# Kernel optimization log

Hardware: AMD Instinct MI355X
Metric: run time of the kernel (lower is better)

The kernel has to match this reference:

```python
import jax, jax.numpy as jnp
import numpy as np

V, D, H, L, F, B, S = 512, 512, 8, 6, 2048, 8, 1024
DK = D // H
EPS = 1e-5


def _positional_encoding(max_len, d_model):
    pos = np.arange(max_len, dtype=np.float32)[:, None]
    div = np.exp(np.arange(0, d_model, 2, dtype=np.float32) * (-np.log(10000.0) / d_model))
    pe = np.zeros((max_len, d_model), dtype=np.float32)
    pe[:, 0::2] = np.sin(pos * div)
    pe[:, 1::2] = np.cos(pos * div)
    return jnp.asarray(pe)


def setup_inputs() -> dict:
    key = jax.random.key(0)
    ks = jax.random.split(key, 24)
    xavier = lambda k, shp: jax.random.normal(k, shp, jnp.float32) * np.sqrt(2.0 / (shp[-2] + shp[-1]))
    inp = {
        "input_ids": jax.random.randint(ks[0], (B, S), 0, V),
        "emb": jax.random.normal(ks[1], (V, D), jnp.float32) * 0.02,
        "pe": _positional_encoding(1024, D),
        "Wq": xavier(ks[2], (L, D, D)), "bq": jnp.zeros((L, D)),
        "Wk": xavier(ks[3], (L, D, D)), "bk": jnp.zeros((L, D)),
        "Wv": xavier(ks[4], (L, D, D)), "bv": jnp.zeros((L, D)),
        "Wo": xavier(ks[5], (L, D, D)), "bo": jnp.zeros((L, D)),
        "ln1_g": jnp.ones((L, D)), "ln1_b": jnp.zeros((L, D)),
        "W1": xavier(ks[6], (L, D, F)), "b1": jnp.zeros((L, F)),
        "W2": xavier(ks[7], (L, F, D)), "b2": jnp.zeros((L, D)),
        "ln2_g": jnp.ones((L, D)), "ln2_b": jnp.zeros((L, D)),
        "Wout": xavier(ks[8], (D, V)), "bout": jnp.zeros((V,)),
    }
    return inp


def _ln(x, g, b):
    mu = jnp.mean(x, -1, keepdims=True)
    var = jnp.mean(jnp.square(x - mu), -1, keepdims=True)
    return (x - mu) * jax.lax.rsqrt(var + EPS) * g + b


def reference(input_ids, emb, pe, Wq, bq, Wk, bk, Wv, bv, Wo, bo,
              ln1_g, ln1_b, W1, b1, W2, b2, ln2_g, ln2_b, Wout, bout):
    h = emb[input_ids] * np.sqrt(D) + pe[:S]  # [B,S,D]
    # Faithful to the original mask bug: masked_fill(mask==0, -1e9) fills the
    # LOWER triangle (incl diagonal); raw scores are kept strictly where j > i.
    r = jnp.arange(S)
    keep = r[None, :] > r[:, None]  # [S,S]

    def block(h, p):
        (wq, bq_, wk, bk_, wv, bv_, wo, bo_,
         g1, be1, w1, b1_, w2, b2_, g2, be2) = p
        split = lambda t: t.reshape(B, S, H, DK).transpose(0, 2, 1, 3)
        q = split(h @ wq + bq_)
        k = split(h @ wk + bk_)
        v = split(h @ wv + bv_)
        scores = jnp.einsum('bhqd,bhkd->bhqk', q, k) / np.sqrt(DK)
        scores = jnp.where(keep, scores, -1e9)
        a = jax.nn.softmax(scores, axis=-1)
        o = jnp.einsum('bhqk,bhkd->bhqd', a, v).transpose(0, 2, 1, 3).reshape(B, S, D)
        h = _ln(h + (o @ wo + bo_), g1, be1)
        f = jax.nn.relu(h @ w1 + b1_) @ w2 + b2_
        h = _ln(h + f, g2, be2)
        return h, None

    params = (Wq, bq, Wk, bk, Wv, bv, Wo, bo, ln1_g, ln1_b, W1, b1, W2, b2, ln2_g, ln2_b)
    h, _ = jax.lax.scan(block, h, params)
    return h @ Wout + bout  # logits [B,S,V]
```

## Files before the change

kernel.cpp:

```cpp
#include <hip/hip_runtime.h>

typedef unsigned short u16;
typedef __attribute__((ext_vector_type(8))) short bf16x8;
typedef __attribute__((ext_vector_type(4))) float f32x4;
typedef __attribute__((ext_vector_type(4))) unsigned int uint4v;
typedef __attribute__((ext_vector_type(4))) unsigned short us4;

#define NLAYER 6
#define D_MODEL 512
#define NHEAD 8
#define DKH 64
#define SEQ 1024
#define BATCH 8
#define FFN 2048
#define MROWS (BATCH * SEQ)
#define QKV_LD 1536
#define SCALE_LOG2E 0.18033688011112042f

__device__ __forceinline__ float b2f(u16 u) {
  union { unsigned u32; float f; } x; x.u32 = ((unsigned)u) << 16; return x.f;
}
__device__ __forceinline__ u16 f2b(float f) {
  union { float f; unsigned u; } x; x.f = f;
  unsigned r = x.u + 0x7FFFu + ((x.u >> 16) & 1u);
  return (u16)(r >> 16);
}
__device__ __forceinline__ void gld16(const u16* g, u16* l) {
  __builtin_amdgcn_global_load_lds(
      (const __attribute__((address_space(1))) unsigned int*)g,
      (__attribute__((address_space(3))) unsigned int*)l, 16, 0, 0);
}

__global__ __launch_bounds__(256) void transpose_cvt_kernel(
    const float* __restrict__ src, u16* __restrict__ dst, int K, int N, size_t dstZ,
    float scale)
{
  __shared__ float t[32][33];
  const int z = blockIdx.z;
  src += (size_t)z * K * N;
  dst += (size_t)z * dstZ;
  const int n0 = blockIdx.x * 32, k0 = blockIdx.y * 32;
  const int tx = threadIdx.x, ty = threadIdx.y;
#pragma unroll
  for (int i = 0; i < 32; i += 8)
    t[ty + i][tx] = src[(size_t)(k0 + ty + i) * N + n0 + tx];
  __syncthreads();
#pragma unroll
  for (int i = 0; i < 32; i += 8)
    dst[(size_t)(n0 + ty + i) * K + k0 + tx] = f2b(t[tx][ty + i] * scale);
}

__global__ __launch_bounds__(256) void concat_bias_kernel(
    const float* __restrict__ bq, const float* __restrict__ bk,
    const float* __restrict__ bv, float* __restrict__ dst)
{
  const int l = blockIdx.x, t = threadIdx.x;
#pragma unroll
  for (int j = t; j < 512; j += 256) {
    dst[l * QKV_LD + j]        = bq[l * 512 + j] * SCALE_LOG2E;
    dst[l * QKV_LD + 512 + j]  = bk[l * 512 + j];
    dst[l * QKV_LD + 1024 + j] = bv[l * 512 + j];
  }
}

__global__ __launch_bounds__(256) void embed_kernel(
    const int* __restrict__ ids, const float* __restrict__ emb,
    const float* __restrict__ pe, float* __restrict__ Hf, u16* __restrict__ Hb)
{
  const int row = blockIdx.x;
  const int s = row & (SEQ - 1);
  const int id = ids[row];
  const int tid = threadIdx.x;
#pragma unroll
  for (int u = 0; u < 2; ++u) {
    const int d = tid + u * 256;
    float v = emb[(size_t)id * D_MODEL + d] * 22.62741699796952f + pe[(size_t)s * D_MODEL + d];
    Hf[(size_t)row * D_MODEL + d] = v;
    Hb[(size_t)row * D_MODEL + d] = f2b(v);
  }
}

template<int BMT, bool RELU, bool OUTF, bool OUTB, bool VT>
__global__ __launch_bounds__(256) void gemm_kernel(
    const u16* __restrict__ A, const u16* __restrict__ Bt,
    const float* __restrict__ bias,
    float* __restrict__ Cf, u16* __restrict__ Cb, u16* __restrict__ Vtp,
    int M, int N, int K)
{
  constexpr int IT = BMT / 32;
  constexpr int AHALF = BMT * 64;
  constexpr int BHALF = 128 * 64;
  __shared__ __align__(16) u16 As[2 * AHALF];
  __shared__ __align__(16) u16 Bs[2 * BHALF];
  const int tid = threadIdx.x;
  const int bm = blockIdx.x * BMT, bn = blockIdx.y * 128;
  const int wave = tid >> 6, lane = tid & 63;
  const int lm = lane & 15, quad = lane >> 4;
  const int wm = (wave & 1) * (BMT / 2), wn = (wave >> 1) * 64;

  const int sr = tid >> 3;
  const int sc = (tid & 7) ^ (sr & 7);
  const u16* Ap = A  + (size_t)(bm + sr) * K + sc * 8;
  const u16* Bp = Bt + (size_t)(bn + sr) * K + sc * 8;
  u16* lA = As + wave * 512;
  u16* lB = Bs + wave * 512;

  f32x4 acc[IT][4] = {};

  const int nt = K >> 6;
  auto stage = [&](int buf, int t) {
    const size_t ko = (size_t)t << 6;
#pragma unroll
    for (int p = 0; p < BMT / 32; ++p)
      gld16(Ap + (size_t)(p * 32) * K + ko, lA + buf * AHALF + p * 2048);
#pragma unroll
    for (int p = 0; p < 4; ++p)
      gld16(Bp + (size_t)(p * 32) * K + ko, lB + buf * BHALF + p * 2048);
  };

  stage(0, 0);
  __syncthreads();

  for (int t = 0; t < nt; ++t) {
    const int cur = t & 1;
    if (t + 1 < nt) stage(cur ^ 1, t + 1);
    const u16* as = As + cur * AHALF;
    const u16* bs = Bs + cur * BHALF;
#pragma unroll
    for (int kh = 0; kh < 2; ++kh) {
      bf16x8 af[IT], bg[4];
#pragma unroll
      for (int i = 0; i < IT; ++i) {
        const int row = wm + i * 16 + lm;
        af[i] = *(const bf16x8*)&as[row * 64 + (((kh * 4 + quad) ^ (row & 7)) << 3)];
      }
#pragma unroll
      for (int j = 0; j < 4; ++j) {
        const int row = wn + j * 16 + lm;
        bg[j] = *(const bf16x8*)&bs[row * 64 + (((kh * 4 + quad) ^ (row & 7)) << 3)];
      }
#pragma unroll
      for (int i = 0; i < IT; ++i)
#pragma unroll
        for (int j = 0; j < 4; ++j)
          acc[i][j] = __builtin_amdgcn_mfma_f32_16x16x32_bf16(af[i], bg[j], acc[i][j], 0, 0, 0);
    }
    __syncthreads();
  }

  const int mbase = bm + wm + quad * 4;
  const int nbase = bn + wn + lm;
#pragma unroll
  for (int i = 0; i < IT; ++i) {
#pragma unroll
    for (int j = 0; j < 4; ++j) {
      const int n = nbase + j * 16;
      const float bv = bias[n];
      float vv[4];
#pragma unroll
      for (int r = 0; r < 4; ++r) {
        float v = acc[i][j][r] + bv;
        if (RELU) v = fmaxf(v, 0.f);
        vv[r] = v;
      }
      if (VT && n >= 1024) {
        const int hh = (n - 1024) >> 6, d = (n - 1024) & 63;
        const int mm = mbase + i * 16;
        const int bb = mm >> 10, ss = mm & 1023;
        us4 pk;
#pragma unroll
        for (int r = 0; r < 4; ++r) pk[r] = f2b(vv[r]);
        *(us4*)&Vtp[(((size_t)(bb * NHEAD + hh)) * 64 + d) * SEQ + ss] = pk;
      } else {
#pragma unroll
        for (int r = 0; r < 4; ++r) {
          const int m = mbase + i * 16 + r;
          if (OUTF) Cf[(size_t)m * N + n] = vv[r];
          if (OUTB) Cb[(size_t)m * N + n] = f2b(vv[r]);
        }
      }
    }
  }
}

__global__ __launch_bounds__(256) void attn_mfma_kernel(
    const u16* __restrict__ QKV, const u16* __restrict__ Vt, u16* __restrict__ O)
{
  __shared__ __align__(16) u16 Ks[64 * 64];
  __shared__ __align__(16) u16 Vs[64 * 64];
  __shared__ __align__(16) u16 Ps[4 * 16 * 64];
  const int tid = threadIdx.x;
  const int wave = tid >> 6, lane = tid & 63;
  const int quad = lane >> 4, l15 = lane & 15;
  const int l7 = l15 & 7;
  const int id = blockIdx.x;
  const int bh = id & 63;
  const int b = bh >> 3, h = bh & 7;
  const int g = id >> 6;
  const int u = g * 4 + wave;
  u16* psw = Ps + wave * (16 * 64);
  const size_t qoff = (size_t)b * SEQ * QKV_LD + h * 64;
  const size_t vtb  = (size_t)bh * 64 * SEQ;

  const int sr = tid >> 3, sc = tid & 7;
  const u16* kg0 = QKV + qoff + 512 + (size_t)sr * QKV_LD + sc * 8;
  const u16* kg1 = kg0 + (size_t)32 * QKV_LD;
  const u16* vg0 = Vt + vtb + (size_t)sr * SEQ + sc * 8;
  const u16* vg1 = vg0 + (size_t)32 * SEQ;
  const int sw = (sc ^ (sr & 7)) << 3;
  u16* ks0 = &Ks[sr * 64 + sw];
  u16* ks1 = &Ks[(sr + 32) * 64 + sw];
  u16* vs0 = &Vs[sr * 64 + sw];
  u16* vs1 = &Vs[(sr + 32) * 64 + sw];

  const u16* qp = QKV + qoff + (size_t)(u * 16 + l15) * QKV_LD + quad * 8;
  const bf16x8 qf0 = *(const bf16x8*)(qp);
  const bf16x8 qf1 = *(const bf16x8*)(qp + 32);

  f32x4 oacc[4] = {};
  float lsum[4] = {0.f, 0.f, 0.f, 0.f};

  uint4v kr0 = *(const uint4v*)(kg0 + (size_t)(g * 64) * QKV_LD);
  uint4v kr1 = *(const uint4v*)(kg1 + (size_t)(g * 64) * QKV_LD);
  uint4v vr0 = *(const uint4v*)(vg0 + g * 64);
  uint4v vr1 = *(const uint4v*)(vg1 + g * 64);

#pragma unroll 1
  for (int jt = g; jt < 16; ++jt) {
    __syncthreads();
    *(uint4v*)ks0 = kr0; *(uint4v*)ks1 = kr1;
    *(uint4v*)vs0 = vr0; *(uint4v*)vs1 = vr1;
    __syncthreads();
    if (jt < 15) {
      kr0 = *(const uint4v*)(kg0 + (size_t)((jt + 1) * 64) * QKV_LD);
      kr1 = *(const uint4v*)(kg1 + (size_t)((jt + 1) * 64) * QKV_LD);
      vr0 = *(const uint4v*)(vg0 + (jt + 1) * 64);
      vr1 = *(const uint4v*)(vg1 + (jt + 1) * 64);
    }
    f32x4 sacc[4] = {};
#pragma unroll
    for (int nt = 0; nt < 4; ++nt) {
      const int key = nt * 16 + l15, k7 = key & 7;
      bf16x8 kb0 = *(const bf16x8*)&Ks[key * 64 + ((quad ^ k7) << 3)];
      bf16x8 kb1 = *(const bf16x8*)&Ks[key * 64 + (((quad + 4) ^ k7) << 3)];
      sacc[nt] = __builtin_amdgcn_mfma_f32_16x16x32_bf16(qf0, kb0, sacc[nt], 0, 0, 0);
      sacc[nt] = __builtin_amdgcn_mfma_f32_16x16x32_bf16(qf1, kb1, sacc[nt], 0, 0, 0);
    }
    const bool diag = (jt == g);
#pragma unroll
    for (int nt = 0; nt < 4; ++nt)
#pragma unroll
      for (int r = 0; r < 4; ++r) {
        float pv = __builtin_amdgcn_exp2f(sacc[nt][r]);
        if (diag) {
          const int i = u * 16 + quad * 4 + r;
          const int j = jt * 64 + nt * 16 + l15;
          pv = (j > i) ? pv : 0.f;
        }
        lsum[r] += pv;
        const int qr = quad * 4 + r;
        const int j2 = nt * 16 + l15;
        psw[qr * 64 + (((j2 >> 3) ^ (qr & 7)) << 3) + (j2 & 7)] = f2b(pv);
      }
    bf16x8 pf0 = *(const bf16x8*)&psw[l15 * 64 + (((quad + 0) ^ l7) << 3)];
    bf16x8 pf1 = *(const bf16x8*)&psw[l15 * 64 + (((quad + 4) ^ l7) << 3)];
#pragma unroll
    for (int nt = 0; nt < 4; ++nt) {
      const int d = nt * 16 + l15, d7 = d & 7;
      bf16x8 vb0 = *(const bf16x8*)&Vs[d * 64 + ((quad ^ d7) << 3)];
      bf16x8 vb1 = *(const bf16x8*)&Vs[d * 64 + (((quad + 4) ^ d7) << 3)];
      oacc[nt] = __builtin_amdgcn_mfma_f32_16x16x32_bf16(pf0, vb0, oacc[nt], 0, 0, 0);
      oacc[nt] = __builtin_amdgcn_mfma_f32_16x16x32_bf16(pf1, vb1, oacc[nt], 0, 0, 0);
    }
  }

#pragma unroll
  for (int o = 1; o < 16; o <<= 1)
#pragma unroll
    for (int r = 0; r < 4; ++r) lsum[r] += __shfl_xor(lsum[r], o, 16);
  float rl[4];
#pragma unroll
  for (int r = 0; r < 4; ++r) rl[r] = 1.0f / lsum[r];
#pragma unroll
  for (int nt = 0; nt < 4; ++nt)
#pragma unroll
    for (int r = 0; r < 4; ++r) {
      const int row = u * 16 + quad * 4 + r;
      O[(size_t)(b * SEQ + row) * D_MODEL + h * DKH + nt * 16 + l15] = f2b(oacc[nt][r] * rl[r]);
    }
}

__global__ __launch_bounds__(256) void vmean_kernel(
    const u16* __restrict__ Vt, u16* __restrict__ O)
{
  const int bh = blockIdx.x, tid = threadIdx.x;
  const int d = tid >> 2, sc = (tid & 3) * 256;
  const u16* p = Vt + ((size_t)bh * 64 + d) * SEQ + sc;
  float s = 0.f;
#pragma unroll 8
  for (int i = 0; i < 256; ++i) s += b2f(p[i]);
  s += __shfl_xor(s, 1, 64);
  s += __shfl_xor(s, 2, 64);
  if ((tid & 3) == 0) {
    const int b = bh >> 3, h = bh & 7;
    O[((size_t)b * SEQ + SEQ - 1) * D_MODEL + h * 64 + d] = f2b(s * (1.f / SEQ));
  }
}

__global__ __launch_bounds__(256) void add_ln_kernel(
    const float* __restrict__ Hin, const u16* __restrict__ T,
    const float* __restrict__ g, const float* __restrict__ bta,
    float* __restrict__ Hout, u16* __restrict__ Hb)
{
  __shared__ float red[8];
  const int row = blockIdx.x, tid = threadIdx.x;
  const int wave = tid >> 6, lane = tid & 63;
  const size_t base = (size_t)row * D_MODEL;
  const float x0 = Hin[base + tid] + b2f(T[base + tid]);
  const float x1 = Hin[base + tid + 256] + b2f(T[base + tid + 256]);
  float s = x0 + x1;
#pragma unroll
  for (int o = 32; o > 0; o >>= 1) s += __shfl_xor(s, o, 64);
  if (lane == 0) red[wave] = s;
  __syncthreads();
  const float mu = (red[0] + red[1] + red[2] + red[3]) * (1.f / 512.f);
  const float d0 = x0 - mu, d1 = x1 - mu;
  float v = d0 * d0 + d1 * d1;
#pragma unroll
  for (int o = 32; o > 0; o >>= 1) v += __shfl_xor(v, o, 64);
  if (lane == 0) red[4 + wave] = v;
  __syncthreads();
  const float var = (red[4] + red[5] + red[6] + red[7]) * (1.f / 512.f);
  const float rs = rsqrtf(var + 1e-5f);
  const float y0 = d0 * rs * g[tid] + bta[tid];
  const float y1 = d1 * rs * g[tid + 256] + bta[tid + 256];
  Hout[base + tid] = y0;
  Hout[base + tid + 256] = y1;
  Hb[base + tid] = f2b(y0);
  Hb[base + tid + 256] = f2b(y1);
}

extern "C" void kernel_launch(void* const* d_in, const int* in_sizes, int n_in,
                              void* d_out, int out_size, void* d_ws, size_t ws_size,
                              hipStream_t stream) {
  (void)in_sizes; (void)n_in; (void)out_size; (void)ws_size;
  const int*   ids  = (const int*)  d_in[0];
  const float* emb  = (const float*)d_in[1];
  const float* pe   = (const float*)d_in[2];
  const float* Wq   = (const float*)d_in[3];
  const float* bq   = (const float*)d_in[4];
  const float* Wk   = (const float*)d_in[5];
  const float* bk   = (const float*)d_in[6];
  const float* Wv   = (const float*)d_in[7];
  const float* bv   = (const float*)d_in[8];
  const float* Wo   = (const float*)d_in[9];
  const float* bo   = (const float*)d_in[10];
  const float* g1   = (const float*)d_in[11];
  const float* be1  = (const float*)d_in[12];
  const float* W1   = (const float*)d_in[13];
  const float* b1   = (const float*)d_in[14];
  const float* W2   = (const float*)d_in[15];
  const float* b2   = (const float*)d_in[16];
  const float* g2   = (const float*)d_in[17];
  const float* be2  = (const float*)d_in[18];
  const float* Wout = (const float*)d_in[19];
  const float* bout = (const float*)d_in[20];
  float* out = (float*)d_out;

  char* wsp = (char*)d_ws;
  auto alloc = [&](size_t bytes) -> char* {
    char* p = wsp; wsp += (bytes + 255) & ~(size_t)255; return p;
  };
  const size_t dd  = (size_t)D_MODEL * D_MODEL;
  const size_t df  = (size_t)D_MODEL * FFN;
  const size_t dq  = (size_t)QKV_LD * D_MODEL;
  u16* wqkv_t = (u16*)alloc(NLAYER * dq * 2);
  u16* wo_t   = (u16*)alloc(NLAYER * dd * 2);
  u16* w1_t   = (u16*)alloc(NLAYER * df * 2);
  u16* w2_t   = (u16*)alloc(NLAYER * df * 2);
  u16* wout_t = (u16*)alloc(dd * 2);
  float* bqkv = (float*)alloc(NLAYER * QKV_LD * 4);
  float* hf   = (float*)alloc((size_t)MROWS * D_MODEL * 4);
  u16*   hb   = (u16*)  alloc((size_t)MROWS * D_MODEL * 2);
  u16*   qkvb = (u16*)  alloc((size_t)MROWS * QKV_LD * 2);
  u16*   ob   = (u16*)  alloc((size_t)MROWS * D_MODEL * 2);
  u16*   vt   = (u16*)  alloc((size_t)BATCH * NHEAD * DKH * SEQ * 2);
  u16*   tb   = (u16*)  alloc((size_t)MROWS * D_MODEL * 2);
  u16*   mid  = qkvb;

  dim3 tb8(32, 8);
  transpose_cvt_kernel<<<dim3(16, 16, NLAYER), tb8, 0, stream>>>(Wq, wqkv_t,            512, 512,  dq, SCALE_LOG2E);
  transpose_cvt_kernel<<<dim3(16, 16, NLAYER), tb8, 0, stream>>>(Wk, wqkv_t + 512*512,  512, 512,  dq, 1.f);
  transpose_cvt_kernel<<<dim3(16, 16, NLAYER), tb8, 0, stream>>>(Wv, wqkv_t + 1024*512, 512, 512,  dq, 1.f);
  transpose_cvt_kernel<<<dim3(16, 16, NLAYER), tb8, 0, stream>>>(Wo, wo_t,   512, 512,  dd, 1.f);
  transpose_cvt_kernel<<<dim3(64, 16, NLAYER), tb8, 0, stream>>>(W1, w1_t,   512, 2048, df, 1.f);
  transpose_cvt_kernel<<<dim3(16, 64, NLAYER), tb8, 0, stream>>>(W2, w2_t,   2048, 512, df, 1.f);
  transpose_cvt_kernel<<<dim3(16, 16, 1),      tb8, 0, stream>>>(Wout, wout_t, 512, 512, dd, 1.f);
  concat_bias_kernel<<<NLAYER, 256, 0, stream>>>(bq, bk, bv, bqkv);

  embed_kernel<<<MROWS, 256, 0, stream>>>(ids, emb, pe, hf, hb);

  for (int l = 0; l < NLAYER; ++l) {
    gemm_kernel<128, false, false, true, true><<<dim3(64, 12), 256, 0, stream>>>(
        hb, wqkv_t + l * dq, bqkv + l * QKV_LD, nullptr, qkvb, vt, MROWS, QKV_LD, 512);
    attn_mfma_kernel<<<1024, 256, 0, stream>>>(qkvb, vt, ob);
    vmean_kernel<<<64, 256, 0, stream>>>(vt, ob);
    gemm_kernel<64, false, false, true, false><<<dim3(128, 4), 256, 0, stream>>>(
        ob, wo_t + l * dd, bo + l * 512, nullptr, tb, nullptr, MROWS, 512, 512);
    add_ln_kernel<<<MROWS, 256, 0, stream>>>(hf, tb, g1 + l * 512, be1 + l * 512, hf, hb);
    gemm_kernel<128, true, false, true, false><<<dim3(64, 16), 256, 0, stream>>>(
        hb, w1_t + l * df, b1 + l * 2048, nullptr, mid, nullptr, MROWS, 2048, 512);
    gemm_kernel<64, false, false, true, false><<<dim3(128, 4), 256, 0, stream>>>(
        mid, w2_t + l * df, b2 + l * 512, nullptr, tb, nullptr, MROWS, 512, 2048);
    add_ln_kernel<<<MROWS, 256, 0, stream>>>(hf, tb, g2 + l * 512, be2 + l * 512, hf, hb);
  }
  gemm_kernel<64, false, true, false, false><<<dim3(128, 4), 256, 0, stream>>>(
      hb, wout_t, bout, out, nullptr, nullptr, MROWS, 512, 512);
}
```

Before: 1.046 ms.

## Add 256x256-tile 8-wave GEMM kernel for QKV and FFN1 projections

Introduces a new GEMM kernel with 256x256 output tiles, 512 threads and double-buffered global-to-LDS direct loads over 128KB of dynamic shared memory. Inside each K-step it splits the MFMA work into four phases that reload A/B fragments between raw barriers, and raises wave priority around the MFMA bursts. The kernel replaces the 128-tile GEMM for the QKV projection and the ReLU FFN1 projection, aiming to raise operand reuse and cut LDS and L2 traffic per flop. In exchange the grids shrink to 192 and 256 blocks with one block per CU, which risks underfilling the GPU and losing latency hiding.

```diff
diff --git a/kernel.cpp b/kernel.cpp
--- a/kernel.cpp
+++ b/kernel.cpp
@@ -30,6 +30,11 @@
       (const __attribute__((address_space(1))) unsigned int*)g,
       (__attribute__((address_space(3))) unsigned int*)l, 16, 0, 0);
 }
+__device__ __forceinline__ void barrier_raw() {
+  asm volatile("" ::: "memory");
+  __builtin_amdgcn_s_barrier();
+  asm volatile("" ::: "memory");
+}
 
 __global__ __launch_bounds__(256) void transpose_cvt_kernel(
     const float* __restrict__ src, u16* __restrict__ dst, int K, int N, size_t dstZ,
@@ -177,6 +182,159 @@
           const int m = mbase + i * 16 + r;
           if (OUTF) Cf[(size_t)m * N + n] = vv[r];
           if (OUTB) Cb[(size_t)m * N + n] = f2b(vv[r]);
+        }
+      }
+    }
+  }
+}
+
+template<bool RELU, bool VT>
+__global__ __launch_bounds__(512, 2) void gemm256_kernel(
+    const u16* __restrict__ A, const u16* __restrict__ Bt,
+    const float* __restrict__ bias,
+    u16* __restrict__ Cb, u16* __restrict__ Vtp,
+    int M, int N, int K)
+{
+  extern __shared__ __align__(16) u16 smem[];
+  u16* Asm = smem;
+  u16* Bsm = smem + 32768;
+  const int tid = threadIdx.x;
+  const int wave = tid >> 6, lane = tid & 63;
+  const int lm = lane & 15, quad = lane >> 4, l7 = lm & 7;
+  const int wm = wave >> 2, wn = wave & 3;
+  const int bm = blockIdx.x * 256, bn = blockIdx.y * 256;
+
+  const int srow = tid >> 3;
+  const int scg = (tid & 7) ^ (srow & 7);
+  const u16* Ap = A  + (size_t)(bm + srow) * K + scg * 8;
+  const u16* Bp = Bt + (size_t)(bn + srow) * K + scg * 8;
+  u16* uA = Asm + wave * 512;
+  u16* uB = Bsm + wave * 512;
+
+  f32x4 acc[8][4] = {};
+
+  const int NT = K >> 6;
+  auto stage = [&](int buf, int t) {
+    const size_t ko = (size_t)t << 6;
+#pragma unroll
+    for (int p = 0; p < 4; ++p)
+      gld16(Ap + (size_t)(p * 64) * K + ko, uA + buf * 16384 + p * 4096);
+#pragma unroll
+    for (int p = 0; p < 4; ++p)
+      gld16(Bp + (size_t)(p * 64) * K + ko, uB + buf * 16384 + p * 4096);
+  };
+
+  stage(0, 0);
+  __syncthreads();
+
+  const int sl0 = (quad ^ l7) << 3;
+  const int sl1 = ((quad + 4) ^ l7) << 3;
+
+#pragma unroll 1
+  for (int t = 0; t < NT; ++t) {
+    const int cur = t & 1;
+    if (t + 1 < NT) stage(cur ^ 1, t + 1);
+    const u16* as_ = Asm + cur * 16384 + (wm * 128 + lm) * 64;
+    const u16* bs_ = Bsm + cur * 16384 + (wn * 64 + lm) * 64;
+    bf16x8 af[4][2], b01[2][2], b23[2][2];
+#pragma unroll
+    for (int i = 0; i < 4; ++i) {
+      af[i][0] = *(const bf16x8*)&as_[i * 1024 + sl0];
+      af[i][1] = *(const bf16x8*)&as_[i * 1024 + sl1];
+    }
+#pragma unroll
+    for (int j = 0; j < 2; ++j) {
+      b01[j][0] = *(const bf16x8*)&bs_[j * 1024 + sl0];
+      b01[j][1] = *(const bf16x8*)&bs_[j * 1024 + sl1];
+    }
+    __builtin_amdgcn_s_setprio(1);
+#pragma unroll
+    for (int i = 0; i < 4; ++i)
+#pragma unroll
+      for (int j = 0; j < 2; ++j) {
+        acc[i][j] = __builtin_amdgcn_mfma_f32_16x16x32_bf16(af[i][0], b01[j][0], acc[i][j], 0, 0, 0);
+        acc[i][j] = __builtin_amdgcn_mfma_f32_16x16x32_bf16(af[i][1], b01[j][1], acc[i][j], 0, 0, 0);
+      }
+    __builtin_amdgcn_s_setprio(0);
+    barrier_raw();
+#pragma unroll
+    for (int j = 0; j < 2; ++j) {
+      b23[j][0] = *(const bf16x8*)&bs_[(j + 2) * 1024 + sl0];
+      b23[j][1] = *(const bf16x8*)&bs_[(j + 2) * 1024 + sl1];
+    }
+    __builtin_amdgcn_s_setprio(1);
+#pragma unroll
+    for (int i = 0; i < 4; ++i)
+#pragma unroll
+      for (int j = 0; j < 2; ++j) {
+        acc[i][j + 2] = __builtin_amdgcn_mfma_f32_16x16x32_bf16(af[i][0], b23[j][0], acc[i][j + 2], 0, 0, 0);
+        acc[i][j + 2] = __builtin_amdgcn_mfma_f32_16x16x32_bf16(af[i][1], b23[j][1], acc[i][j + 2], 0, 0, 0);
+      }
+    __builtin_amdgcn_s_setprio(0);
+    barrier_raw();
+#pragma unroll
+    for (int i = 0; i < 4; ++i) {
+      af[i][0] = *(const bf16x8*)&as_[(i + 4) * 1024 + sl0];
+      af[i][1] = *(const bf16x8*)&as_[(i + 4) * 1024 + sl1];
+    }
+    __builtin_amdgcn_s_setprio(1);
+#pragma unroll
+    for (int i = 0; i < 4; ++i)
+#pragma unroll
+      for (int j = 0; j < 2; ++j) {
+        acc[i + 4][j + 2] = __builtin_amdgcn_mfma_f32_16x16x32_bf16(af[i][0], b23[j][0], acc[i + 4][j + 2], 0, 0, 0);
+        acc[i + 4][j + 2] = __builtin_amdgcn_mfma_f32_16x16x32_bf16(af[i][1], b23[j][1], acc[i + 4][j + 2], 0, 0, 0);
+      }
+    __builtin_amdgcn_s_setprio(0);
+    barrier_raw();
+#pragma unroll
+    for (int j = 0; j < 2; ++j) {
+      b01[j][0] = *(const bf16x8*)&bs_[j * 1024 + sl0];
+      b01[j][1] = *(const bf16x8*)&bs_[j * 1024 + sl1];
+    }
+    __builtin_amdgcn_s_setprio(1);
+#pragma unroll
+    for (int i = 0; i < 4; ++i)
+#pragma unroll
+      for (int j = 0; j < 2; ++j) {
+        acc[i + 4][j] = __builtin_amdgcn_mfma_f32_16x16x32_bf16(af[i][0], b01[j][0], acc[i + 4][j], 0, 0, 0);
+        acc[i + 4][j] = __builtin_amdgcn_mfma_f32_16x16x32_bf16(af[i][1], b01[j][1], acc[i + 4][j], 0, 0, 0);
+      }
+    __builtin_amdgcn_s_setprio(0);
+    if (t + 1 < NT) {
+      asm volatile("s_waitcnt vmcnt(0)" ::: "memory");
+      barrier_raw();
+    }
+  }
+
+  const int mbase = bm + wm * 128 + quad * 4;
+  const int nbase = bn + wn * 64 + lm;
+#pragma unroll
+  for (int i = 0; i < 8; ++i) {
+#pragma unroll
+    for (int j = 0; j < 4; ++j) {
+      const int n = nbase + j * 16;
+      const float bv = bias[n];
+      float vv[4];
+#pragma unroll
+      for (int r = 0; r < 4; ++r) {
+        float v = acc[i][j][r] + bv;
+        if (RELU) v = fmaxf(v, 0.f);
+        vv[r] = v;
+      }
+      if (VT && n >= 1024) {
+        const int hh = (n - 1024) >> 6, d = (n - 1024) & 63;
+        const int mm = mbase + i * 16;
+        const int bb = mm >> 10, ss = mm & 1023;
+        us4 pk;
+#pragma unroll
+        for (int r = 0; r < 4; ++r) pk[r] = f2b(vv[r]);
+        *(us4*)&Vtp[(((size_t)(bb * NHEAD + hh)) * 64 + d) * SEQ + ss] = pk;
+      } else {
+#pragma unroll
+        for (int r = 0; r < 4; ++r) {
+          const int m = mbase + i * 16 + r;
+          Cb[(size_t)m * N + n] = f2b(vv[r]);
         }
       }
     }
@@ -367,6 +525,15 @@
   const float* bout = (const float*)d_in[20];
   float* out = (float*)d_out;
 
+  static int attr_set = 0;
+  if (!attr_set) {
+    hipFuncSetAttribute(reinterpret_cast<const void*>(&gemm256_kernel<false, true>),
+                        hipFuncAttributeMaxDynamicSharedMemorySize, 131072);
+    hipFuncSetAttribute(reinterpret_cast<const void*>(&gemm256_kernel<true, false>),
+                        hipFuncAttributeMaxDynamicSharedMemorySize, 131072);
+    attr_set = 1;
+  }
+
   char* wsp = (char*)d_ws;
   auto alloc = [&](size_t bytes) -> char* {
     char* p = wsp; wsp += (bytes + 255) & ~(size_t)255; return p;
@@ -401,15 +568,15 @@
   embed_kernel<<<MROWS, 256, 0, stream>>>(ids, emb, pe, hf, hb);
 
   for (int l = 0; l < NLAYER; ++l) {
-    gemm_kernel<128, false, false, true, true><<<dim3(64, 12), 256, 0, stream>>>(
-        hb, wqkv_t + l * dq, bqkv + l * QKV_LD, nullptr, qkvb, vt, MROWS, QKV_LD, 512);
+    gemm256_kernel<false, true><<<dim3(32, 6), 512, 131072, stream>>>(
+        hb, wqkv_t + l * dq, bqkv + l * QKV_LD, qkvb, vt, MROWS, QKV_LD, 512);
     attn_mfma_kernel<<<1024, 256, 0, stream>>>(qkvb, vt, ob);
     vmean_kernel<<<64, 256, 0, stream>>>(vt, ob);
     gemm_kernel<64, false, false, true, false><<<dim3(128, 4), 256, 0, stream>>>(
         ob, wo_t + l * dd, bo + l * 512, nullptr, tb, nullptr, MROWS, 512, 512);
     add_ln_kernel<<<MROWS, 256, 0, stream>>>(hf, tb, g1 + l * 512, be1 + l * 512, hf, hb);
-    gemm_kernel<128, true, false, true, false><<<dim3(64, 16), 256, 0, stream>>>(
-        hb, w1_t + l * df, b1 + l * 2048, nullptr, mid, nullptr, MROWS, 2048, 512);
+    gemm256_kernel<true, false><<<dim3(32, 8), 512, 131072, stream>>>(
+        hb, w1_t + l * df, b1 + l * 2048, mid, nullptr, MROWS, 2048, 512);
     gemm_kernel<64, false, false, true, false><<<dim3(128, 4), 256, 0, stream>>>(
         mid, w2_t + l * df, b2 + l * 512, nullptr, tb, nullptr, MROWS, 512, 2048);
     add_ln_kernel<<<MROWS, 256, 0, stream>>>(hf, tb, g2 + l * 512, be2 + l * 512, hf, hb);
```

Result: no change. 1.026 ms (-1.9%).
